# Performance work log

Hardware: AMD Instinct MI355X
Metric: run time of the kernel (lower is better)

## Reference

```python
import jax, jax.numpy as jnp
import numpy as np

NUM_EXPERTS = 8
CAPACITY = 320  # per-batch per-expert token capacity


def setup_inputs() -> dict:
    key = jax.random.key(0)
    k0, k1, k2, k3 = jax.random.split(key, 4)
    B, S, D, F = 4, 2048, 1024, 4096
    E = NUM_EXPERTS
    hidden_states = jax.random.normal(k0, (B, S, D), dtype=jnp.float32)
    gate_w = jax.random.normal(k1, (E, D), dtype=jnp.float32) * 0.02
    w1 = jax.random.normal(k2, (E, D, F), dtype=jnp.float32) * 0.02
    w2 = jax.random.normal(k3, (E, F, D), dtype=jnp.float32) * 0.02
    return {"hidden_states": hidden_states, "gate_w": gate_w, "w1": w1, "w2": w2}


def reference(hidden_states, gate_w, w1, w2):
    E, C = NUM_EXPERTS, CAPACITY
    B, S, D = hidden_states.shape

    # --- route ---
    router_logits = jnp.einsum('bsd,ed->bse', hidden_states, gate_w)
    router_probs = jax.nn.softmax(router_logits, axis=-1)
    expert_idx = jnp.argmax(router_probs, axis=-1)                      # [B,S]
    onehot = jax.nn.one_hot(expert_idx, E, dtype=jnp.int32)             # [B,S,E]
    priority = jnp.cumsum(onehot, axis=1)                               # [B,S,E]
    router_mask = onehot * (priority <= C)                              # [B,S,E]
    assigned = jnp.sum(router_mask, axis=-1) > 0                        # [B,S]
    # slot within expert buffer; dropped tokens go to overflow slot C
    slot = jnp.where(assigned, jnp.sum(priority * onehot, axis=-1) - 1, C)  # [B,S]
    top_prob = jnp.max(router_probs, axis=-1, keepdims=True)            # [B,S,1]

    # --- dispatch: scatter tokens into [B,E,C+1,D] buffers ---
    def dispatch(x_b, e_b, s_b):
        return jnp.zeros((E, C + 1, D), x_b.dtype).at[e_b, s_b].set(x_b)
    buf = jax.vmap(dispatch)(hidden_states, expert_idx, slot)           # [B,E,C+1,D]

    # --- per-expert FFN as grouped GEMM ---
    h = jax.nn.silu(jnp.einsum('becd,edf->becf', buf, w1))
    y = jnp.einsum('becf,efd->becd', h, w2)                             # [B,E,C+1,D]

    # --- combine: gather expert outputs back to token order ---
    gathered = jax.vmap(lambda y_b, e_b, s_b: y_b[e_b, s_b])(y, expert_idx, slot)  # [B,S,D]
    next_states = jnp.where(assigned[..., None], gathered, hidden_states)
    out = top_prob * next_states

    # argmax of capacity-masked one-hot: dropped tokens -> expert 0
    expert_index = jnp.where(assigned, expert_idx, 0)
    return out, router_logits, expert_index
```

## Files before the change

kernel.cpp:

```cpp
#include <hip/hip_runtime.h>

#define B_  4
#define S_  2048
#define D_  1024
#define F_  4096
#define E_  8
#define C_  320
#define MPAD_ 1280
#define NT_ (B_*S_)

typedef short bf16x8 __attribute__((ext_vector_type(8)));
typedef float f32x4  __attribute__((ext_vector_type(4)));

using gptr_t = const __attribute__((address_space(1))) void*;
using lptr_t = __attribute__((address_space(3))) void*;

__device__ static inline void gll16(const void* g, void* l) {
    __builtin_amdgcn_global_load_lds((gptr_t)g, (lptr_t)l, 16, 0, 0);
}

__device__ static inline unsigned short f2b(float f) {
    unsigned int u = __float_as_uint(f);
    u += 0x7fffu + ((u >> 16) & 1u);
    return (unsigned short)(u >> 16);
}

__global__ __launch_bounds__(256) void k_convT(const float* __restrict__ in,
                                               unsigned short* __restrict__ out,
                                               int R, int Cc) {
    __shared__ unsigned short ld[64][66];
    int e = blockIdx.z;
    const float* src = in + (size_t)e * R * Cc;
    unsigned short* dst = out + (size_t)e * R * Cc;
    int c0 = blockIdx.x * 64, r0 = blockIdx.y * 64;
    int t = threadIdx.x;

    int rr = t >> 4;
    int cg = t & 15;
#pragma unroll
    for (int p = 0; p < 4; p++) {
        int row = p * 16 + rr;
        float4 v = *(const float4*)(src + (size_t)(r0 + row) * Cc + c0 + cg * 4);
        ld[cg * 4 + 0][row] = f2b(v.x);
        ld[cg * 4 + 1][row] = f2b(v.y);
        ld[cg * 4 + 2][row] = f2b(v.z);
        ld[cg * 4 + 3][row] = f2b(v.w);
    }
    __syncthreads();

    int cc = t >> 3;
    int rg = t & 7;
#pragma unroll
    for (int p = 0; p < 2; p++) {
        int col = p * 32 + cc;
        const unsigned* lp = (const unsigned*)&ld[col][rg * 8];
        uint4 w;
        w.x = lp[0]; w.y = lp[1]; w.z = lp[2]; w.w = lp[3];
        *(uint4*)(dst + (size_t)(c0 + col) * R + r0 + rg * 8) = w;
    }
}

__global__ __launch_bounds__(256) void k_router(const float* __restrict__ hs,
                                                const float* __restrict__ gw,
                                                float* __restrict__ logits,
                                                int* __restrict__ eidx,
                                                float* __restrict__ tp) {
    int tok  = (int)((blockIdx.x * 256 + threadIdx.x) >> 6);
    int lane = threadIdx.x & 63;
    const float* x = hs + (size_t)tok * D_;
    double acc[E_];
#pragma unroll
    for (int e = 0; e < E_; e++) acc[e] = 0.0;
    for (int i = 0; i < 16; i++) {
        float xv = x[lane + 64 * i];
#pragma unroll
        for (int e = 0; e < E_; e++)
            acc[e] += (double)xv * (double)gw[e * D_ + lane + 64 * i];
    }
#pragma unroll
    for (int e = 0; e < E_; e++) {
#pragma unroll
        for (int off = 32; off > 0; off >>= 1)
            acc[e] += __shfl_xor(acc[e], off, 64);
    }
    if (lane == 0) {
        float l[E_];
        float mx = -1e30f; int am = 0;
#pragma unroll
        for (int e = 0; e < E_; e++) {
            l[e] = (float)acc[e];
            if (l[e] > mx) { mx = l[e]; am = e; }
        }
        float se = 0.f;
#pragma unroll
        for (int e = 0; e < E_; e++) se += __expf(l[e] - mx);
        tp[tok]   = 1.0f / se;
        eidx[tok] = am;
#pragma unroll
        for (int e = 0; e < E_; e++) logits[(size_t)tok * E_ + e] = l[e];
    }
}

__global__ __launch_bounds__(256) void k_scan(const int* __restrict__ eidx,
                                              int* __restrict__ slot,
                                              int* __restrict__ tok_list,
                                              int* __restrict__ counts,
                                              float* __restrict__ eif) {
    int b = blockIdx.x;
    __shared__ int cCnt[32][E_];
    __shared__ int cBase[32][E_];
    int t = threadIdx.x, wv = t >> 6, lane = t & 63;
    const int* eb = eidx + b * S_;
    for (int c = wv; c < 32; c += 4) {
        int e = eb[c * 64 + lane];
#pragma unroll
        for (int x = 0; x < E_; x++) {
            unsigned long long m = __ballot(e == x);
            if (lane == 0) cCnt[c][x] = __popcll(m);
        }
    }
    __syncthreads();
    if (t < E_) {
        int s = 0;
        for (int c = 0; c < 32; c++) { cBase[c][t] = s; s += cCnt[c][t]; }
        counts[b * E_ + t] = s;
    }
    __syncthreads();
    for (int c = wv; c < 32; c += 4) {
        int s_tok = c * 64 + lane;
        int e = eb[s_tok];
        unsigned long long lowmask = (1ull << lane) - 1ull;
        int rank = 0;
#pragma unroll
        for (int x = 0; x < E_; x++) {
            unsigned long long m = __ballot(e == x);
            if (x == e) rank = __popcll(m & lowmask);
        }
        int pos = cBase[c][e] + rank;
        int assigned = (pos < C_);
        slot[b * S_ + s_tok] = assigned ? pos : C_;
        if (assigned) tok_list[(b * E_ + e) * C_ + pos] = s_tok;
        eif[b * S_ + s_tok] = assigned ? (float)e : 0.0f;
    }
}

__global__ void k_base(const int* __restrict__ counts,
                       int* __restrict__ ebase,
                       int* __restrict__ nE) {
    int e = threadIdx.x;
    if (e < E_) {
        int s = 0;
#pragma unroll
        for (int b = 0; b < B_; b++) {
            ebase[b * E_ + e] = s;
            s += min(counts[b * E_ + e], C_);
        }
        nE[e] = s;
    }
}

__global__ __launch_bounds__(256) void k_dispatch(const float* __restrict__ hs,
                                                  const int* __restrict__ tlB,
                                                  const int* __restrict__ ebase,
                                                  const int* __restrict__ nE,
                                                  int* __restrict__ tlG,
                                                  unsigned short* __restrict__ Xd) {
    int w    = (int)((blockIdx.x * 256 + threadIdx.x) >> 6);
    int lane = threadIdx.x & 63;
    int e = w / MPAD_, r = w - e * MPAD_;
    unsigned short* drow = Xd + ((size_t)e * MPAD_ + r) * D_;
    if (r < nE[e]) {
        int b = 0;
#pragma unroll
        for (int bb = 1; bb < B_; bb++) if (r >= ebase[bb * E_ + e]) b = bb;
        int pos = r - ebase[b * E_ + e];
        int ts  = tlB[(b * E_ + e) * C_ + pos];
        if (lane == 0) tlG[e * MPAD_ + r] = b * S_ + ts;
        const float* src = hs + ((size_t)b * S_ + ts) * D_;
#pragma unroll
        for (int i = 0; i < 2; i++) {
            int c0 = (lane + 64 * i) * 8;
            float4 v0 = *(const float4*)(src + c0);
            float4 v1 = *(const float4*)(src + c0 + 4);
            uint4 pk;
            pk.x = (unsigned)f2b(v0.x) | ((unsigned)f2b(v0.y) << 16);
            pk.y = (unsigned)f2b(v0.z) | ((unsigned)f2b(v0.w) << 16);
            pk.z = (unsigned)f2b(v1.x) | ((unsigned)f2b(v1.y) << 16);
            pk.w = (unsigned)f2b(v1.z) | ((unsigned)f2b(v1.w) << 16);
            *(uint4*)(drow + c0) = pk;
        }
    } else {
        uint4 zz = {0u, 0u, 0u, 0u};
#pragma unroll
        for (int i = 0; i < 2; i++)
            *(uint4*)(drow + (lane + 64 * i) * 8) = zz;
    }
}

template<int LDK, int KT>
__device__ __forceinline__ void gemm_core(const unsigned short* __restrict__ Ab,
                                          const unsigned short* __restrict__ Bb,
                                          char* sm, f32x4 (&acc)[4][4]) {
    const int t    = threadIdx.x;
    const int lane = t & 63;
    const int wv   = t >> 6;
    const int wm   = wv >> 1;
    const int wn   = wv & 1;

    const int sr  = t >> 3;
    const int scs = (t & 7) ^ (sr & 7);
    const unsigned short* aS = Ab + (size_t)sr * LDK + scs * 8;
    const unsigned short* bS = Bb + (size_t)sr * LDK + scs * 8;
    char* ldsA = sm;
    char* ldsB = sm + 16384;
    const int wvoff = wv * 1024;

    const int rl  = lane & 15;
    const int sw  = lane & 7;
    const int kg  = lane >> 4;
    const int sx0 = ((kg    ) ^ sw) << 4;
    const int sx1 = ((kg + 4) ^ sw) << 4;
    const int aro = (wm * 64 + rl) * 128;
    const int bro = (wn * 64 + rl) * 128;

#pragma unroll 1
    for (int kt = 0; kt < KT; ++kt) {
        __syncthreads();
        const unsigned short* aP = aS + kt * 64;
        const unsigned short* bP = bS + kt * 64;
#pragma unroll
        for (int j = 0; j < 4; j++) gll16(aP + (size_t)(j * 32) * LDK, ldsA + j * 4096 + wvoff);
#pragma unroll
        for (int j = 0; j < 4; j++) gll16(bP + (size_t)(j * 32) * LDK, ldsB + j * 4096 + wvoff);
        __syncthreads();

        bf16x8 a[4], b[4];
#pragma unroll
        for (int i = 0; i < 4; i++) a[i] = *(const bf16x8*)(ldsA + aro + i * 2048 + sx0);
#pragma unroll
        for (int j = 0; j < 4; j++) b[j] = *(const bf16x8*)(ldsB + bro + j * 2048 + sx0);
#pragma unroll
        for (int i = 0; i < 4; i++)
#pragma unroll
            for (int j = 0; j < 4; j++)
                acc[i][j] = __builtin_amdgcn_mfma_f32_16x16x32_bf16(a[i], b[j], acc[i][j], 0, 0, 0);
#pragma unroll
        for (int i = 0; i < 4; i++) a[i] = *(const bf16x8*)(ldsA + aro + i * 2048 + sx1);
#pragma unroll
        for (int j = 0; j < 4; j++) b[j] = *(const bf16x8*)(ldsB + bro + j * 2048 + sx1);
#pragma unroll
        for (int i = 0; i < 4; i++)
#pragma unroll
            for (int j = 0; j < 4; j++)
                acc[i][j] = __builtin_amdgcn_mfma_f32_16x16x32_bf16(a[i], b[j], acc[i][j], 0, 0, 0);
    }
}

__global__ __launch_bounds__(256, 4) void k_ffn1(const unsigned short* __restrict__ Xd,
                                                 const unsigned short* __restrict__ w1t,
                                                 const int* __restrict__ nE,
                                                 unsigned short* __restrict__ h) {
    __shared__ __align__(16) char sm[32768];
    int id  = blockIdx.x;
    int e   = id & 7;
    int rem = id >> 3;
    int mt  = rem % 10;
    int nt  = rem / 10;
    int m0  = mt * 128;
    if (m0 >= nE[e]) return;
    int n0  = nt * 128;

    f32x4 acc[4][4];
    f32x4 z = {0.f, 0.f, 0.f, 0.f};
#pragma unroll
    for (int i = 0; i < 4; i++)
#pragma unroll
        for (int j = 0; j < 4; j++) acc[i][j] = z;

    const unsigned short* Ab = Xd  + ((size_t)e * MPAD_ + m0) * D_;
    const unsigned short* Bb = w1t + ((size_t)e * F_    + n0) * D_;
    gemm_core<D_, D_ / 64>(Ab, Bb, sm, acc);

    int lane = threadIdx.x & 63, wv = threadIdx.x >> 6, wm = wv >> 1, wn = wv & 1;
    unsigned short* hb = h + (size_t)e * MPAD_ * F_;
    int rb = m0 + wm * 64 + ((lane >> 4) << 2);
    int cb = n0 + wn * 64 + (lane & 15);
#pragma unroll
    for (int i = 0; i < 4; i++)
#pragma unroll
        for (int r = 0; r < 4; r++) {
            unsigned short* hr = hb + (size_t)(rb + i * 16 + r) * F_ + cb;
#pragma unroll
            for (int j = 0; j < 4; j++) {
                float v = acc[i][j][r];
                v = v / (1.0f + __expf(-v));
                hr[j * 16] = f2b(v);
            }
        }
}

__global__ __launch_bounds__(256, 4) void k_ffn2(const unsigned short* __restrict__ h,
                                                 const unsigned short* __restrict__ w2t,
                                                 const int* __restrict__ nE,
                                                 const int* __restrict__ tlG,
                                                 const float* __restrict__ tp,
                                                 float* __restrict__ out) {
    __shared__ __align__(16) char sm[32768];
    int id  = blockIdx.x;
    int e   = id & 7;
    int rem = id >> 3;
    int mt  = rem % 10;
    int nt  = rem / 10;
    int m0  = mt * 128;
    int n   = nE[e];
    if (m0 >= n) return;
    int n0  = nt * 128;

    f32x4 acc[4][4];
    f32x4 z = {0.f, 0.f, 0.f, 0.f};
#pragma unroll
    for (int i = 0; i < 4; i++)
#pragma unroll
        for (int j = 0; j < 4; j++) acc[i][j] = z;

    const unsigned short* Ab = h   + ((size_t)e * MPAD_ + m0) * F_;
    const unsigned short* Bb = w2t + ((size_t)e * D_    + n0) * F_;
    gemm_core<F_, F_ / 64>(Ab, Bb, sm, acc);

    int lane = threadIdx.x & 63, wv = threadIdx.x >> 6, wm = wv >> 1, wn = wv & 1;
    const int* tl = tlG + e * MPAD_;
    int rb = m0 + wm * 64 + ((lane >> 4) << 2);
    int cb = n0 + wn * 64 + (lane & 15);
#pragma unroll
    for (int i = 0; i < 4; i++)
#pragma unroll
        for (int r = 0; r < 4; r++) {
            int row = rb + i * 16 + r;
            if (row < n) {
                int gt = tl[row];
                float sc = tp[gt];
                float* orow = out + (size_t)gt * D_ + cb;
#pragma unroll
                for (int j = 0; j < 4; j++)
                    orow[j * 16] = sc * acc[i][j][r];
            }
        }
}

__global__ __launch_bounds__(256) void k_pass(const float* __restrict__ hs,
                                              const int* __restrict__ slot,
                                              const float* __restrict__ tp,
                                              float* __restrict__ out) {
    int tok  = (int)((blockIdx.x * 256 + threadIdx.x) >> 6);
    int lane = threadIdx.x & 63;
    if (slot[tok] < C_) return;
    float sc = tp[tok];
    const float* src = hs + (size_t)tok * D_;
    float* dst = out + (size_t)tok * D_;
#pragma unroll
    for (int i = 0; i < 4; i++) {
        float4 v = *(const float4*)(src + (lane + 64 * i) * 4);
        v.x *= sc; v.y *= sc; v.z *= sc; v.w *= sc;
        *(float4*)(dst + (lane + 64 * i) * 4) = v;
    }
}

extern "C" void kernel_launch(void* const* d_in, const int* in_sizes, int n_in,
                              void* d_out, int out_size, void* d_ws, size_t ws_size,
                              hipStream_t stream) {
    const float* hs = (const float*)d_in[0];
    const float* gw = (const float*)d_in[1];
    const float* w1 = (const float*)d_in[2];
    const float* w2 = (const float*)d_in[3];

    float* out    = (float*)d_out;
    float* logits = out + (size_t)NT_ * D_;
    float* eif    = logits + (size_t)NT_ * E_;

    char* ws = (char*)d_ws;
    int*            eidx   = (int*)(ws + 0);
    int*            slot   = (int*)(ws + 65536);
    float*          tp     = (float*)(ws + 131072);
    int*            tlB    = (int*)(ws + 196608);
    int*            tlG    = (int*)(ws + 237568);
    int*            counts = (int*)(ws + 278528);
    int*            ebase  = (int*)(ws + 278784);
    int*            nE     = (int*)(ws + 279040);
    unsigned short* Xd     = (unsigned short*)(ws + 327680);
    unsigned short* w1t    = (unsigned short*)(ws + 33554432ull);
    unsigned short* w2t    = (unsigned short*)(ws + 100663296ull);
    unsigned short* hbuf   = (unsigned short*)(ws + 167772160ull);

    dim3 blk(256);
    k_convT<<<dim3(F_ / 64, D_ / 64, E_), blk, 0, stream>>>(w1, w1t, D_, F_);
    k_convT<<<dim3(D_ / 64, F_ / 64, E_), blk, 0, stream>>>(w2, w2t, F_, D_);
    k_router<<<dim3(NT_ / 4), blk, 0, stream>>>(hs, gw, logits, eidx, tp);
    k_scan<<<dim3(B_), blk, 0, stream>>>(eidx, slot, tlB, counts, eif);
    k_base<<<dim3(1), dim3(64), 0, stream>>>(counts, ebase, nE);
    k_dispatch<<<dim3(E_ * MPAD_ / 4), blk, 0, stream>>>(hs, tlB, ebase, nE, tlG, Xd);
    k_ffn1<<<dim3(2560), blk, 0, stream>>>(Xd, w1t, nE, hbuf);
    k_ffn2<<<dim3(640), blk, 0, stream>>>(hbuf, w2t, nE, tlG, tp, out);
    k_pass<<<dim3(NT_ / 4), blk, 0, stream>>>(hs, slot, tp, out);
}
```

Measured before the change: 536.2 us.

## Merge weight conversion, router, base computation and passthrough into fewer launches

Folds both weight transpose-convert kernels and the router into one mega kernel selected by block index, computes per-expert bases inside dispatch instead of a separate launch, and appends passthrough blocks to the FFN2 grid. This cuts launch count from nine to five and lets independent work share a grid. The FFN kernels' launch bounds are also raised to 5 blocks per CU, which caps registers harder and may cause spills. Every dispatch wave now recomputes the bases redundantly.

```diff
diff --git a/kernel.cpp b/kernel.cpp
--- a/kernel.cpp
+++ b/kernel.cpp
@@ -25,48 +25,59 @@
     return (unsigned short)(u >> 16);
 }
 
-__global__ __launch_bounds__(256) void k_convT(const float* __restrict__ in,
-                                               unsigned short* __restrict__ out,
-                                               int R, int Cc) {
+__global__ __launch_bounds__(256) void k_mega(const float* __restrict__ w1,
+                                              const float* __restrict__ w2,
+                                              unsigned short* __restrict__ w1t,
+                                              unsigned short* __restrict__ w2t,
+                                              const float* __restrict__ hs,
+                                              const float* __restrict__ gw,
+                                              float* __restrict__ logits,
+                                              int* __restrict__ eidx,
+                                              float* __restrict__ tp) {
     __shared__ unsigned short ld[64][66];
-    int e = blockIdx.z;
-    const float* src = in + (size_t)e * R * Cc;
-    unsigned short* dst = out + (size_t)e * R * Cc;
-    int c0 = blockIdx.x * 64, r0 = blockIdx.y * 64;
+    int bid = blockIdx.x;
     int t = threadIdx.x;
 
-    int rr = t >> 4;
-    int cg = t & 15;
-#pragma unroll
-    for (int p = 0; p < 4; p++) {
-        int row = p * 16 + rr;
-        float4 v = *(const float4*)(src + (size_t)(r0 + row) * Cc + c0 + cg * 4);
-        ld[cg * 4 + 0][row] = f2b(v.x);
-        ld[cg * 4 + 1][row] = f2b(v.y);
-        ld[cg * 4 + 2][row] = f2b(v.z);
-        ld[cg * 4 + 3][row] = f2b(v.w);
-    }
-    __syncthreads();
-
-    int cc = t >> 3;
-    int rg = t & 7;
-#pragma unroll
-    for (int p = 0; p < 2; p++) {
-        int col = p * 32 + cc;
-        const unsigned* lp = (const unsigned*)&ld[col][rg * 8];
-        uint4 w;
-        w.x = lp[0]; w.y = lp[1]; w.z = lp[2]; w.w = lp[3];
-        *(uint4*)(dst + (size_t)(c0 + col) * R + r0 + rg * 8) = w;
-    }
-}
-
-__global__ __launch_bounds__(256) void k_router(const float* __restrict__ hs,
-                                                const float* __restrict__ gw,
-                                                float* __restrict__ logits,
-                                                int* __restrict__ eidx,
-                                                float* __restrict__ tp) {
-    int tok  = (int)((blockIdx.x * 256 + threadIdx.x) >> 6);
-    int lane = threadIdx.x & 63;
+    if (bid < 16384) {
+        const float* src; unsigned short* dst; int R, Cc, c0, r0;
+        if (bid < 8192) {
+            int e = bid >> 10, rem = bid & 1023;
+            R = D_; Cc = F_;
+            c0 = (rem & 63) * 64; r0 = (rem >> 6) * 64;
+            src = w1 + (size_t)e * R * Cc; dst = w1t + (size_t)e * R * Cc;
+        } else {
+            int b2 = bid - 8192;
+            int e = b2 >> 10, rem = b2 & 1023;
+            R = F_; Cc = D_;
+            c0 = (rem & 15) * 64; r0 = (rem >> 4) * 64;
+            src = w2 + (size_t)e * R * Cc; dst = w2t + (size_t)e * R * Cc;
+        }
+        int rr = t >> 4, cg = t & 15;
+#pragma unroll
+        for (int p = 0; p < 4; p++) {
+            int row = p * 16 + rr;
+            float4 v = *(const float4*)(src + (size_t)(r0 + row) * Cc + c0 + cg * 4);
+            ld[cg * 4 + 0][row] = f2b(v.x);
+            ld[cg * 4 + 1][row] = f2b(v.y);
+            ld[cg * 4 + 2][row] = f2b(v.z);
+            ld[cg * 4 + 3][row] = f2b(v.w);
+        }
+        __syncthreads();
+        int cc = t >> 3, rg = t & 7;
+#pragma unroll
+        for (int p = 0; p < 2; p++) {
+            int col = p * 32 + cc;
+            const unsigned* lp = (const unsigned*)&ld[col][rg * 8];
+            uint4 w;
+            w.x = lp[0]; w.y = lp[1]; w.z = lp[2]; w.w = lp[3];
+            *(uint4*)(dst + (size_t)(c0 + col) * R + r0 + rg * 8) = w;
+        }
+        return;
+    }
+
+    int rb = bid - 16384;
+    int tok  = (int)((rb * 256 + t) >> 6);
+    int lane = t & 63;
     const float* x = hs + (size_t)tok * D_;
     double acc[E_];
 #pragma unroll
@@ -144,36 +155,31 @@
     }
 }
 
-__global__ void k_base(const int* __restrict__ counts,
-                       int* __restrict__ ebase,
-                       int* __restrict__ nE) {
-    int e = threadIdx.x;
-    if (e < E_) {
-        int s = 0;
-#pragma unroll
-        for (int b = 0; b < B_; b++) {
-            ebase[b * E_ + e] = s;
-            s += min(counts[b * E_ + e], C_);
-        }
-        nE[e] = s;
-    }
-}
-
 __global__ __launch_bounds__(256) void k_dispatch(const float* __restrict__ hs,
                                                   const int* __restrict__ tlB,
-                                                  const int* __restrict__ ebase,
-                                                  const int* __restrict__ nE,
+                                                  const int* __restrict__ counts,
+                                                  int* __restrict__ nE,
                                                   int* __restrict__ tlG,
                                                   unsigned short* __restrict__ Xd) {
     int w    = (int)((blockIdx.x * 256 + threadIdx.x) >> 6);
     int lane = threadIdx.x & 63;
     int e = w / MPAD_, r = w - e * MPAD_;
+
+    int ebv[B_]; int s = 0;
+#pragma unroll
+    for (int bb = 0; bb < B_; bb++) {
+        ebv[bb] = s;
+        s += min(counts[bb * E_ + e], C_);
+    }
+    int ne = s;
+    if (r == 0 && lane == 0) nE[e] = ne;
+
     unsigned short* drow = Xd + ((size_t)e * MPAD_ + r) * D_;
-    if (r < nE[e]) {
+    if (r < ne) {
         int b = 0;
 #pragma unroll
-        for (int bb = 1; bb < B_; bb++) if (r >= ebase[bb * E_ + e]) b = bb;
-        int pos = r - ebase[b * E_ + e];
+        for (int bb = 1; bb < B_; bb++) if (r >= ebv[bb]) b = bb;
+        int pos = r - ebv[b];
         int ts  = tlB[(b * E_ + e) * C_ + pos];
         if (lane == 0) tlG[e * MPAD_ + r] = b * S_ + ts;
         const float* src = hs + ((size_t)b * S_ + ts) * D_;
@@ -256,7 +262,7 @@
     }
 }
 
-__global__ __launch_bounds__(256, 4) void k_ffn1(const unsigned short* __restrict__ Xd,
+__global__ __launch_bounds__(256, 5) void k_ffn1(const unsigned short* __restrict__ Xd,
                                                  const unsigned short* __restrict__ w1t,
                                                  const int* __restrict__ nE,
                                                  unsigned short* __restrict__ h) {
@@ -299,14 +305,37 @@
         }
 }
 
-__global__ __launch_bounds__(256, 4) void k_ffn2(const unsigned short* __restrict__ h,
+__global__ __launch_bounds__(256, 5) void k_ffn2(const unsigned short* __restrict__ h,
                                                  const unsigned short* __restrict__ w2t,
                                                  const int* __restrict__ nE,
                                                  const int* __restrict__ tlG,
                                                  const float* __restrict__ tp,
+                                                 const int* __restrict__ slot,
+                                                 const float* __restrict__ hs,
                                                  float* __restrict__ out) {
     __shared__ __align__(16) char sm[32768];
     int id  = blockIdx.x;
+
+    if (id >= 640) {
+        int pb = id - 640;
+        int wv = threadIdx.x >> 6, lane = threadIdx.x & 63;
+        int base = pb * 64 + wv * 16;
+        for (int k = 0; k < 16; k++) {
+            int tok = base + k;
+            if (slot[tok] < C_) continue;
+            float sc = tp[tok];
+            const float* src = hs + (size_t)tok * D_;
+            float* dst = out + (size_t)tok * D_;
+#pragma unroll
+            for (int i = 0; i < 4; i++) {
+                float4 v = *(const float4*)(src + (lane + 64 * i) * 4);
+                v.x *= sc; v.y *= sc; v.z *= sc; v.w *= sc;
+                *(float4*)(dst + (lane + 64 * i) * 4) = v;
+            }
+        }
+        return;
+    }
+
     int e   = id & 7;
     int rem = id >> 3;
     int mt  = rem % 10;
@@ -347,24 +376,6 @@
         }
 }
 
-__global__ __launch_bounds__(256) void k_pass(const float* __restrict__ hs,
-                                              const int* __restrict__ slot,
-                                              const float* __restrict__ tp,
-                                              float* __restrict__ out) {
-    int tok  = (int)((blockIdx.x * 256 + threadIdx.x) >> 6);
-    int lane = threadIdx.x & 63;
-    if (slot[tok] < C_) return;
-    float sc = tp[tok];
-    const float* src = hs + (size_t)tok * D_;
-    float* dst = out + (size_t)tok * D_;
-#pragma unroll
-    for (int i = 0; i < 4; i++) {
-        float4 v = *(const float4*)(src + (lane + 64 * i) * 4);
-        v.x *= sc; v.y *= sc; v.z *= sc; v.w *= sc;
-        *(float4*)(dst + (lane + 64 * i) * 4) = v;
-    }
-}
-
 extern "C" void kernel_launch(void* const* d_in, const int* in_sizes, int n_in,
                               void* d_out, int out_size, void* d_ws, size_t ws_size,
                               hipStream_t stream) {
@@ -384,7 +395,6 @@
     int*            tlB    = (int*)(ws + 196608);
     int*            tlG    = (int*)(ws + 237568);
     int*            counts = (int*)(ws + 278528);
-    int*            ebase  = (int*)(ws + 278784);
     int*            nE     = (int*)(ws + 279040);
     unsigned short* Xd     = (unsigned short*)(ws + 327680);
     unsigned short* w1t    = (unsigned short*)(ws + 33554432ull);
@@ -392,13 +402,9 @@
     unsigned short* hbuf   = (unsigned short*)(ws + 167772160ull);
 
     dim3 blk(256);
-    k_convT<<<dim3(F_ / 64, D_ / 64, E_), blk, 0, stream>>>(w1, w1t, D_, F_);
-    k_convT<<<dim3(D_ / 64, F_ / 64, E_), blk, 0, stream>>>(w2, w2t, F_, D_);
-    k_router<<<dim3(NT_ / 4), blk, 0, stream>>>(hs, gw, logits, eidx, tp);
+    k_mega<<<dim3(18432), blk, 0, stream>>>(w1, w2, w1t, w2t, hs, gw, logits, eidx, tp);
     k_scan<<<dim3(B_), blk, 0, stream>>>(eidx, slot, tlB, counts, eif);
-    k_base<<<dim3(1), dim3(64), 0, stream>>>(counts, ebase, nE);
-    k_dispatch<<<dim3(E_ * MPAD_ / 4), blk, 0, stream>>>(hs, tlB, ebase, nE, tlG, Xd);
+    k_dispatch<<<dim3(E_ * MPAD_ / 4), blk, 0, stream>>>(hs, tlB, counts, nE, tlG, Xd);
     k_ffn1<<<dim3(2560), blk, 0, stream>>>(Xd, w1t, nE, hbuf);
-    k_ffn2<<<dim3(640), blk, 0, stream>>>(hbuf, w2t, nE, tlG, tp, out);
-    k_pass<<<dim3(NT_ / 4), blk, 0, stream>>>(hs, slot, tp, out);
-}
+    k_ffn2<<<dim3(768), blk, 0, stream>>>(hbuf, w2t, nE, tlG, tp, slot, hs, out);
+}
```

After: 533.2 us. Within noise of the previous version (-0.6%).
